# Performance work log

Measured on AMD Instinct MI355X. Metric: run time of the kernel, lower is better.

## Reference

```python
import jax, jax.numpy as jnp
import numpy as np

N = 50000
E = 800000
IN_DIM = 128
HEADS = 4
OUT_DIM = 32
TOT = HEADS * OUT_DIM  # 128 == IN_DIM -> residual_proj is None
LN_EPS = 1e-5
NEG_SLOPE = 0.2


def setup_inputs() -> dict:
    key = jax.random.key(0)
    ks = jax.random.split(key, 10)
    x = jax.random.normal(ks[0], (N, IN_DIM), dtype=jnp.float32)
    # random edges guaranteed src != dst (PyG GATv2Conv removes then re-adds self loops)
    src = jax.random.randint(ks[1], (E,), 0, N)
    off = jax.random.randint(ks[2], (E,), 1, N)
    dst = (src + off) % N
    edge_index = jnp.stack([src, dst]).astype(jnp.int64)
    # glorot-style init for weights
    sc = 1.0 / np.sqrt(IN_DIM)
    W_l = jax.random.uniform(ks[3], (IN_DIM, TOT), jnp.float32, -sc, sc)
    b_l = jnp.zeros((TOT,), jnp.float32)
    W_r = jax.random.uniform(ks[4], (IN_DIM, TOT), jnp.float32, -sc, sc)
    b_r = jnp.zeros((TOT,), jnp.float32)
    att = jax.random.uniform(ks[5], (HEADS, OUT_DIM), jnp.float32, -sc, sc)
    bias = jnp.zeros((TOT,), jnp.float32)
    ln_g = jnp.ones((TOT,), jnp.float32)
    ln_b = jnp.zeros((TOT,), jnp.float32)
    return {"x": x, "edge_index": edge_index, "W_l": W_l, "b_l": b_l,
            "W_r": W_r, "b_r": b_r, "att": att, "bias": bias,
            "ln_g": ln_g, "ln_b": ln_b}


def _gatv2_layer(x, src, dst, W_l, b_l, W_r, b_r, att, bias, ln_g, ln_b):
    n = x.shape[0]
    # GATv2Conv: x_l = lin_l(x) (source/messages), x_r = lin_r(x) (target)
    xl = (x @ W_l + b_l).reshape(n, HEADS, OUT_DIM)
    xr = (x @ W_r + b_r).reshape(n, HEADS, OUT_DIM)
    m = xl[src] + xr[dst]                               # [E+N, H, D]
    s = jnp.einsum('ehd,hd->eh', jax.nn.leaky_relu(m, NEG_SLOPE), att)
    # per-destination softmax (every node has a self loop -> no empty segments)
    smax = jax.ops.segment_max(s, dst, num_segments=n)  # [N, H]
    e = jnp.exp(s - smax[dst])
    denom = jax.ops.segment_sum(e, dst, num_segments=n)
    alpha = e / denom[dst]                              # [E+N, H]
    out = jax.ops.segment_sum(alpha[..., None] * xl[src], dst, num_segments=n)
    out = out.reshape(n, TOT) + bias
    out = out + x                                       # residual (in_dim == total_out_dim)
    mu = jnp.mean(out, axis=-1, keepdims=True)
    var = jnp.mean(jnp.square(out - mu), axis=-1, keepdims=True)
    y = (out - mu) / jnp.sqrt(var + LN_EPS) * ln_g + ln_b
    return jax.nn.elu(y)


def reference(x, edge_index, W_l, b_l, W_r, b_r, att, bias, ln_g, ln_b):
    n = x.shape[0]
    loops = jnp.arange(n, dtype=edge_index.dtype)
    src = jnp.concatenate([edge_index[0], loops])
    dst = jnp.concatenate([edge_index[1], loops])
    return _gatv2_layer(x, src, dst, W_l, b_l, W_r, b_r, att, bias, ln_g, ln_b)
```

## Files before the change

kernel.cpp:

```cpp
#include <hip/hip_runtime.h>

#define N_NODES 50000
#define E_EDGES 800000
#define M_TOTAL (E_EDGES + N_NODES)
#define IN_DIM 128
#define HEADS 4
#define OUT_DIM 32
#define TOT 128
#define LN_EPS 1e-5f
#define NEG_SLOPE 0.2f

#define SCAN_NBLK ((N_NODES + 255) / 256)
#define GEMM_NBLK ((N_NODES + 63) / 64)
#define CHUNK_NBLK ((M_TOTAL / 4 + 255) / 256)
#define HIST_NBLK 64
#define EPB 13312
#define HALF 25000

typedef __bf16 bf16x8 __attribute__((ext_vector_type(8)));
typedef float  f32x4  __attribute__((ext_vector_type(4)));
typedef _Float16 h2   __attribute__((ext_vector_type(2)));

__device__ __forceinline__ float quad_sum(float p) {
    p += __int_as_float(__builtin_amdgcn_update_dpp(
        0, __float_as_int(p), 0xB1 , 0xF, 0xF, true));
    p += __int_as_float(__builtin_amdgcn_update_dpp(
        0, __float_as_int(p), 0x4E , 0xF, 0xF, true));
    return p;
}

__global__ __launch_bounds__(256) void wthist_kernel(
    const int* __restrict__ dsts,
    const float* __restrict__ Wl, const float* __restrict__ Wr,
    unsigned* __restrict__ WT, unsigned char* __restrict__ H,
    unsigned char* __restrict__ rank8) {
    __shared__ unsigned cnt[HALF / 2];
    const int b = blockIdx.x, t = threadIdx.x;
    if (b < 64) {
        const int u = b * 256 + t;
        const int col = u >> 6, k2 = u & 63;
        const float* __restrict__ W = (col < 128) ? Wl : Wr;
        const int c = col & 127;
        union { __bf16 bb[2]; unsigned uu; } p;
        p.bb[0] = (__bf16)W[(2 * k2) * TOT + c];
        p.bb[1] = (__bf16)W[(2 * k2 + 1) * TOT + c];
        WT[col * 64 + k2] = p.uu;
        return;
    }
    const int hb = b - 64;
    const int m_begin = hb * EPB;
    const int m_end = min(m_begin + EPB, M_TOTAL);
    for (int pass = 0; pass < 2; ++pass) {
        const int lo = pass * HALF;
        for (int i = t; i < HALF / 2; i += 256) cnt[i] = 0;
        __syncthreads();
        for (int m0 = m_begin + t * 4; m0 < m_end; m0 += 1024) {
            int d[4];
            if (m0 < E_EDGES) {
                const int4 dv = *(const int4*)&dsts[m0];
                d[0] = dv.x; d[1] = dv.y; d[2] = dv.z; d[3] = dv.w;
            } else {
                d[0] = m0 - E_EDGES; d[1] = d[0] + 1; d[2] = d[0] + 2; d[3] = d[0] + 3;
            }
#pragma unroll
            for (int k = 0; k < 4; ++k) {
                const int dd = d[k] - lo;
                if ((unsigned)dd < (unsigned)HALF) {
                    const int sh = (dd & 1) * 16;
                    const unsigned old = atomicAdd(&cnt[dd >> 1], 1u << sh);
                    rank8[m0 + k] = (unsigned char)((old >> sh) & 0xffffu);
                }
            }
        }
        __syncthreads();
        unsigned* __restrict__ Hrow = (unsigned*)(H + (size_t)hb * N_NODES + lo);
        for (int i = t; i < HALF / 4; i += 256) {
            const unsigned w0 = cnt[2 * i], w1 = cnt[2 * i + 1];
            Hrow[i] = (w0 & 0xffu) | (((w0 >> 16) & 0xffu) << 8) |
                      ((w1 & 0xffu) << 16) | (((w1 >> 16) & 0xffu) << 24);
        }
        __syncthreads();
    }
}

__global__ __launch_bounds__(256) void scan1_kernel(
    const unsigned char* __restrict__ H, unsigned char* __restrict__ P,
    int* __restrict__ incl, int* __restrict__ blockSums,
    int* __restrict__ degtot) {
    __shared__ int sh[256];
    const int t = threadIdx.x;
    const int i = blockIdx.x * 256 + t;
    int tot = 0;
    if (i < N_NODES) {
        int run = 0;
#pragma unroll
        for (int b = 0; b < HIST_NBLK; ++b) {
            const int h = H[(size_t)b * N_NODES + i];
            P[(size_t)b * N_NODES + i] = (unsigned char)run;
            run += h;
        }
        tot = run;
        degtot[i] = tot;
    }
    sh[t] = tot;
    __syncthreads();
#pragma unroll
    for (int off = 1; off < 256; off <<= 1) {
        int u = (t >= off) ? sh[t - off] : 0;
        __syncthreads();
        sh[t] += u;
        __syncthreads();
    }
    if (i < N_NODES) incl[i] = sh[t];
    if (t == 255) blockSums[blockIdx.x] = sh[255];
}

__global__ __launch_bounds__(256) void scan23_kernel(
    const int* __restrict__ degtot, const int* __restrict__ blockSums,
    int* __restrict__ rowptr ) {
    __shared__ int sh[256];
    const int t = threadIdx.x;
    const int v0 = (t < SCAN_NBLK) ? blockSums[t] : 0;
    sh[t] = v0;
    __syncthreads();
#pragma unroll
    for (int off = 1; off < 256; off <<= 1) {
        int u = (t >= off) ? sh[t - off] : 0;
        __syncthreads();
        sh[t] += u;
        __syncthreads();
    }
    const int blockOff = (blockIdx.x == 0) ? 0 : sh[blockIdx.x - 1];
    const int i = blockIdx.x * 256 + t;
    if (i < N_NODES)
        rowptr[i] = blockOff + rowptr[i] - degtot[i];
    if (i == 0) rowptr[N_NODES] = M_TOTAL;
}

__global__ __launch_bounds__(256) void scattergemm_kernel(
    const int* __restrict__ srcs, const int* __restrict__ dsts,
    const int* __restrict__ rowptr, const unsigned char* __restrict__ P,
    const unsigned char* __restrict__ rank8,
    unsigned short* __restrict__ sorted16,
    const float* __restrict__ x, const unsigned* __restrict__ WT,
    const float* __restrict__ bl, const float* __restrict__ br,
    unsigned* __restrict__ xlb, unsigned* __restrict__ xrb) {
    if (blockIdx.x >= GEMM_NBLK) {
        const int sb = blockIdx.x - GEMM_NBLK;
        const int m0 = (sb * 256 + threadIdx.x) * 4;
        if (m0 >= M_TOTAL) return;
        int s[4], d[4];
        if (m0 < E_EDGES) {
            const int4 sv = *(const int4*)&srcs[m0];
            const int4 dv = *(const int4*)&dsts[m0];
            s[0] = sv.x; s[1] = sv.y; s[2] = sv.z; s[3] = sv.w;
            d[0] = dv.x; d[1] = dv.y; d[2] = dv.z; d[3] = dv.w;
        } else {
            s[0] = d[0] = m0 - E_EDGES;
            s[1] = d[1] = d[0] + 1; s[2] = d[2] = d[0] + 2; s[3] = d[3] = d[0] + 3;
        }
        const int hb = m0 / EPB;
        const unsigned char* __restrict__ Pb = P + (size_t)hb * N_NODES;
        const uchar4 r = *(const uchar4*)&rank8[m0];
        sorted16[rowptr[d[0]] + (int)Pb[d[0]] + (int)r.x] = (unsigned short)s[0];
        sorted16[rowptr[d[1]] + (int)Pb[d[1]] + (int)r.y] = (unsigned short)s[1];
        sorted16[rowptr[d[2]] + (int)Pb[d[2]] + (int)r.z] = (unsigned short)s[2];
        sorted16[rowptr[d[3]] + (int)Pb[d[3]] + (int)r.w] = (unsigned short)s[3];
        return;
    }
    __shared__ float epi[4][16][66];
    const int t = threadIdx.x, w = t >> 6, lane = t & 63;
    const int q = lane >> 4, ln = lane & 15;
    const int m0 = blockIdx.x * 64;

    const int row = min(m0 + w * 16 + ln, N_NODES - 1);
    const float* __restrict__ xrow = x + (size_t)row * IN_DIM;
    bf16x8 A[4];
#pragma unroll
    for (int c = 0; c < 4; ++c) {
        const float4 v0 = *(const float4*)&xrow[c * 32 + q * 8];
        const float4 v1 = *(const float4*)&xrow[c * 32 + q * 8 + 4];
        bf16x8 a;
        a[0] = (__bf16)v0.x; a[1] = (__bf16)v0.y; a[2] = (__bf16)v0.z; a[3] = (__bf16)v0.w;
        a[4] = (__bf16)v1.x; a[5] = (__bf16)v1.y; a[6] = (__bf16)v1.z; a[7] = (__bf16)v1.w;
        A[c] = a;
    }

    const int mr = lane >> 2, cg2 = (lane & 3) * 16;
    const int grow = m0 + w * 16 + mr;
#pragma unroll
    for (int g = 0; g < 4; ++g) {
        const int n0 = g * 64;
        const float* __restrict__ bvec = (g < 2) ? bl : br;
        f32x4 acc[4];
#pragma unroll
        for (int nt = 0; nt < 4; ++nt) {
            const float b = bvec[(n0 & 127) + nt * 16 + ln];
            acc[nt] = (f32x4){b, b, b, b};
        }
#pragma unroll
        for (int nt = 0; nt < 4; ++nt) {
            const int col = n0 + nt * 16 + ln;
#pragma unroll
            for (int c = 0; c < 4; ++c) {
                const bf16x8 B = *(const bf16x8*)&WT[col * 64 + c * 16 + q * 4];
                acc[nt] = __builtin_amdgcn_mfma_f32_16x16x32_bf16(A[c], B, acc[nt], 0, 0, 0);
            }
        }
#pragma unroll
        for (int nt = 0; nt < 4; ++nt)
#pragma unroll
            for (int r = 0; r < 4; ++r)
                epi[w][q * 4 + r][nt * 16 + ln] = acc[nt][r];

        if (grow < N_NODES) {
            unsigned p[8];
#pragma unroll
            for (int i = 0; i < 8; ++i) {
                union { _Float16 h[2]; unsigned u; } pk;
                pk.h[0] = (_Float16)epi[w][mr][cg2 + 2 * i];
                pk.h[1] = (_Float16)epi[w][mr][cg2 + 2 * i + 1];
                p[i] = pk.u;
            }
            unsigned* __restrict__ dst = ((g < 2) ? xlb : xrb) +
                (size_t)grow * 64 + (g & 1) * 32 + (cg2 >> 1);
            *(uint4*)&dst[0] = make_uint4(p[0], p[1], p[2], p[3]);
            *(uint4*)&dst[4] = make_uint4(p[4], p[5], p[6], p[7]);
        }
    }
}

__global__ __launch_bounds__(256) void gat_kernel(
    const int* __restrict__ rowptr, const unsigned short* __restrict__ sorted16,
    const unsigned* __restrict__ xlb, const unsigned* __restrict__ xrb,
    const float* __restrict__ att, const float* __restrict__ x,
    const float* __restrict__ bias, const float* __restrict__ g,
    const float* __restrict__ bvec, float* __restrict__ out) {
    const int d = blockIdx.x * 4 + (threadIdx.x >> 6);
    const int lane = threadIdx.x & 63;
    const int ln = lane & 15, q = lane >> 4;
    if (d >= N_NODES) return;

    h2 xrh[4], ath[4];
    {
        const uint4 ur = *(const uint4*)&xrb[(size_t)d * 64 + 4 * ln];
        union { uint4 u; h2 h[4]; } cr; cr.u = ur;
        xrh[0] = cr.h[0]; xrh[1] = cr.h[1]; xrh[2] = cr.h[2]; xrh[3] = cr.h[3];
        const float4 a0 = *(const float4*)&att[8 * ln];
        const float4 a1 = *(const float4*)&att[8 * ln + 4];
        ath[0][0] = (_Float16)a0.x; ath[0][1] = (_Float16)a0.y;
        ath[1][0] = (_Float16)a0.z; ath[1][1] = (_Float16)a0.w;
        ath[2][0] = (_Float16)a1.x; ath[2][1] = (_Float16)a1.y;
        ath[3][0] = (_Float16)a1.z; ath[3][1] = (_Float16)a1.w;
    }
    const h2 slope = (h2){(_Float16)NEG_SLOPE, (_Float16)NEG_SLOPE};
    const int beg = rowptr[d], end = rowptr[d + 1];

    float l = 0.f;
    h2 acc4[4];
#pragma unroll
    for (int k = 0; k < 4; ++k) acc4[k] = (h2){(_Float16)0.f, (_Float16)0.f};

    int s_b = (int)sorted16[min(beg + 4 + q, end - 1)];
    uint4 u;
    {
        const int s_a = (int)sorted16[min(beg + q, end - 1)];
        u = *(const uint4*)&xlb[(size_t)s_a * 64 + 4 * ln];
    }

    for (int base = beg; base < end; base += 4) {
        const int s_c = (int)sorted16[min(base + 8 + q, end - 1)];
        const uint4 u_next = *(const uint4*)&xlb[(size_t)s_b * 64 + 4 * ln];

        const bool valid = (base + q) < end;
        union { unsigned uu; h2 h; } c0, c1, c2, c3;
        c0.uu = u.x; c1.uu = u.y; c2.uu = u.z; c3.uu = u.w;
        h2 m0 = c0.h + xrh[0], m1 = c1.h + xrh[1];
        h2 m2 = c2.h + xrh[2], m3 = c3.h + xrh[3];
        m0 = __builtin_elementwise_max(m0, m0 * slope);
        m1 = __builtin_elementwise_max(m1, m1 * slope);
        m2 = __builtin_elementwise_max(m2, m2 * slope);
        m3 = __builtin_elementwise_max(m3, m3 * slope);
        float p = __builtin_amdgcn_fdot2(m0, ath[0], 0.0f, false);
        p = __builtin_amdgcn_fdot2(m1, ath[1], p, false);
        p = __builtin_amdgcn_fdot2(m2, ath[2], p, false);
        p = __builtin_amdgcn_fdot2(m3, ath[3], p, false);
        p = quad_sum(p);
        const float e = valid ? __expf(p) : 0.f;
        l += e;
        const _Float16 eh = (_Float16)e;
        const h2 e2 = (h2){eh, eh};
        acc4[0] += e2 * c0.h;
        acc4[1] += e2 * c1.h;
        acc4[2] += e2 * c2.h;
        acc4[3] += e2 * c3.h;

        u = u_next; s_b = s_c;
    }

#pragma unroll
    for (int off = 16; off <= 32; off <<= 1) {
        l += __shfl_xor(l, off, 64);
#pragma unroll
        for (int k = 0; k < 4; ++k) {
            union { h2 h; int i; } tmp; tmp.h = acc4[k];
            tmp.i = __shfl_xor(tmp.i, off, 64);
            acc4[k] += tmp.h;
        }
    }
    float acc[8];
#pragma unroll
    for (int k = 0; k < 4; ++k) {
        acc[2 * k]     = (float)acc4[k][0];
        acc[2 * k + 1] = (float)acc4[k][1];
    }

    const float inv_l = 1.0f / l;
    const float4 xv0 = *(const float4*)&x[(size_t)d * TOT + 8 * ln];
    const float4 xv1 = *(const float4*)&x[(size_t)d * TOT + 8 * ln + 4];
    const float4 bi0 = *(const float4*)&bias[8 * ln];
    const float4 bi1 = *(const float4*)&bias[8 * ln + 4];
    float v[8];
    v[0] = fmaf(acc[0], inv_l, bi0.x + xv0.x);
    v[1] = fmaf(acc[1], inv_l, bi0.y + xv0.y);
    v[2] = fmaf(acc[2], inv_l, bi0.z + xv0.z);
    v[3] = fmaf(acc[3], inv_l, bi0.w + xv0.w);
    v[4] = fmaf(acc[4], inv_l, bi1.x + xv1.x);
    v[5] = fmaf(acc[5], inv_l, bi1.y + xv1.y);
    v[6] = fmaf(acc[6], inv_l, bi1.z + xv1.z);
    v[7] = fmaf(acc[7], inv_l, bi1.w + xv1.w);
    float sum = 0.f, sq = 0.f;
#pragma unroll
    for (int k = 0; k < 8; ++k) { sum += v[k]; sq = fmaf(v[k], v[k], sq); }
#pragma unroll
    for (int off = 1; off <= 8; off <<= 1) {
        sum += __shfl_xor(sum, off, 64);
        sq  += __shfl_xor(sq,  off, 64);
    }
    const float mu  = sum * (1.0f / TOT);
    const float var = sq * (1.0f / TOT) - mu * mu;
    const float inv = rsqrtf(var + LN_EPS);
    const float4 g0 = *(const float4*)&g[8 * ln];
    const float4 g1 = *(const float4*)&g[8 * ln + 4];
    const float4 b0 = *(const float4*)&bvec[8 * ln];
    const float4 b1 = *(const float4*)&bvec[8 * ln + 4];
    float y[8];
    y[0] = (v[0] - mu) * inv * g0.x + b0.x;
    y[1] = (v[1] - mu) * inv * g0.y + b0.y;
    y[2] = (v[2] - mu) * inv * g0.z + b0.z;
    y[3] = (v[3] - mu) * inv * g0.w + b0.w;
    y[4] = (v[4] - mu) * inv * g1.x + b1.x;
    y[5] = (v[5] - mu) * inv * g1.y + b1.y;
    y[6] = (v[6] - mu) * inv * g1.z + b1.z;
    y[7] = (v[7] - mu) * inv * g1.w + b1.w;
#pragma unroll
    for (int k = 0; k < 8; ++k) y[k] = y[k] > 0.f ? y[k] : __expf(y[k]) - 1.f;
    if (q < 2) {
        float4 o = (q == 0) ? make_float4(y[0], y[1], y[2], y[3])
                            : make_float4(y[4], y[5], y[6], y[7]);
        *(float4*)&out[(size_t)d * TOT + 8 * ln + 4 * q] = o;
    }
}

extern "C" void kernel_launch(void* const* d_in, const int* in_sizes, int n_in,
                              void* d_out, int out_size, void* d_ws, size_t ws_size,
                              hipStream_t stream) {
    const float* x    = (const float*)d_in[0];
    const int*   ei   = (const int*)d_in[1];
    const float* Wl   = (const float*)d_in[2];
    const float* bl   = (const float*)d_in[3];
    const float* Wr   = (const float*)d_in[4];
    const float* br   = (const float*)d_in[5];
    const float* att  = (const float*)d_in[6];
    const float* bias = (const float*)d_in[7];
    const float* ln_g = (const float*)d_in[8];
    const float* ln_b = (const float*)d_in[9];
    const int* srcs = ei;
    const int* dsts = ei + E_EDGES;

    unsigned* xlb = (unsigned*)d_ws;
    unsigned* xrb = xlb + (size_t)N_NODES * 64;
    int*   degtot     = (int*)(xrb + (size_t)N_NODES * 64);
    int*   rowptr     = degtot + N_NODES;
    int*   blockSums  = rowptr + N_NODES + 1;
    unsigned* WT      = (unsigned*)(blockSums + SCAN_NBLK + 3);
    unsigned char* H  = (unsigned char*)(WT + 256 * 64);
    unsigned char* P  = H + (size_t)HIST_NBLK * N_NODES;
    unsigned short* sorted16 = (unsigned short*)(P + (size_t)HIST_NBLK * N_NODES);
    unsigned char*  rank8    = (unsigned char*)(sorted16 + M_TOTAL);

    wthist_kernel<<<64 + HIST_NBLK, 256, 0, stream>>>(dsts, Wl, Wr, WT, H, rank8);
    scan1_kernel<<<SCAN_NBLK, 256, 0, stream>>>(H, P, rowptr, blockSums, degtot);
    scan23_kernel<<<SCAN_NBLK, 256, 0, stream>>>(degtot, blockSums, rowptr);
    scattergemm_kernel<<<GEMM_NBLK + CHUNK_NBLK, 256, 0, stream>>>(
        srcs, dsts, rowptr, P, rank8, sorted16, x, WT, bl, br, xlb, xrb);
    gat_kernel<<<(N_NODES + 3) / 4, 256, 0, stream>>>(rowptr, sorted16, xlb, xrb, att, x,
                                                      bias, ln_g, ln_b, (float*)d_out);
}
```

Measured before the change: 195.5 us.

## Use 8-bit packed single-pass histogram, in-place scan, and 2x-unrolled edge loop

The histogram kernel now packs four 8-bit counters per LDS word, so all 50000 nodes fit in one pass instead of two 16-bit passes. The block count doubles to keep per-block counts below 256. The scan overwrites the histogram in place, dropping the separate P buffer. The gather loop in the attention kernel processes two groups of four edges per iteration with deeper prefetch, giving more memory-level parallelism. The costs are a larger LDS footprint (lower occupancy for the histogram blocks), twice as many histogram rows to scan, and higher register pressure in the gather loop.

```diff
diff --git a/kernel.cpp b/kernel.cpp
--- a/kernel.cpp
+++ b/kernel.cpp
@@ -13,9 +13,8 @@
 #define SCAN_NBLK ((N_NODES + 255) / 256)
 #define GEMM_NBLK ((N_NODES + 63) / 64)
 #define CHUNK_NBLK ((M_TOTAL / 4 + 255) / 256)
-#define HIST_NBLK 64
-#define EPB 13312
-#define HALF 25000
+#define HIST_NBLK 128
+#define EPB 6656
 
 typedef __bf16 bf16x8 __attribute__((ext_vector_type(8)));
 typedef float  f32x4  __attribute__((ext_vector_type(4)));
@@ -32,9 +31,9 @@
 __global__ __launch_bounds__(256) void wthist_kernel(
     const int* __restrict__ dsts,
     const float* __restrict__ Wl, const float* __restrict__ Wr,
-    unsigned* __restrict__ WT, unsigned char* __restrict__ H,
+    unsigned* __restrict__ WT, unsigned char* __restrict__ HP,
     unsigned char* __restrict__ rank8) {
-    __shared__ unsigned cnt[HALF / 2];
+    __shared__ unsigned cnt[N_NODES / 4];
     const int b = blockIdx.x, t = threadIdx.x;
     if (b < 64) {
         const int u = b * 256 + t;
@@ -50,41 +49,35 @@
     const int hb = b - 64;
     const int m_begin = hb * EPB;
     const int m_end = min(m_begin + EPB, M_TOTAL);
-    for (int pass = 0; pass < 2; ++pass) {
-        const int lo = pass * HALF;
-        for (int i = t; i < HALF / 2; i += 256) cnt[i] = 0;
-        __syncthreads();
-        for (int m0 = m_begin + t * 4; m0 < m_end; m0 += 1024) {
-            int d[4];
-            if (m0 < E_EDGES) {
-                const int4 dv = *(const int4*)&dsts[m0];
-                d[0] = dv.x; d[1] = dv.y; d[2] = dv.z; d[3] = dv.w;
-            } else {
-                d[0] = m0 - E_EDGES; d[1] = d[0] + 1; d[2] = d[0] + 2; d[3] = d[0] + 3;
-            }
-#pragma unroll
-            for (int k = 0; k < 4; ++k) {
-                const int dd = d[k] - lo;
-                if ((unsigned)dd < (unsigned)HALF) {
-                    const int sh = (dd & 1) * 16;
-                    const unsigned old = atomicAdd(&cnt[dd >> 1], 1u << sh);
-                    rank8[m0 + k] = (unsigned char)((old >> sh) & 0xffffu);
-                }
-            }
-        }
-        __syncthreads();
-        unsigned* __restrict__ Hrow = (unsigned*)(H + (size_t)hb * N_NODES + lo);
-        for (int i = t; i < HALF / 4; i += 256) {
-            const unsigned w0 = cnt[2 * i], w1 = cnt[2 * i + 1];
-            Hrow[i] = (w0 & 0xffu) | (((w0 >> 16) & 0xffu) << 8) |
-                      ((w1 & 0xffu) << 16) | (((w1 >> 16) & 0xffu) << 24);
-        }
-        __syncthreads();
-    }
+    for (int i = t; i < N_NODES / 4; i += 256) cnt[i] = 0;
+    __syncthreads();
+    for (int m0 = m_begin + t * 4; m0 < m_end; m0 += 1024) {
+        int d[4];
+        if (m0 < E_EDGES) {
+            const int4 dv = *(const int4*)&dsts[m0];
+            d[0] = dv.x; d[1] = dv.y; d[2] = dv.z; d[3] = dv.w;
+        } else {
+            d[0] = m0 - E_EDGES; d[1] = d[0] + 1; d[2] = d[0] + 2; d[3] = d[0] + 3;
+        }
+        uchar4 r;
+        unsigned old, sh;
+        sh = (d[0] & 3) * 8; old = atomicAdd(&cnt[d[0] >> 2], 1u << sh);
+        r.x = (unsigned char)(old >> sh);
+        sh = (d[1] & 3) * 8; old = atomicAdd(&cnt[d[1] >> 2], 1u << sh);
+        r.y = (unsigned char)(old >> sh);
+        sh = (d[2] & 3) * 8; old = atomicAdd(&cnt[d[2] >> 2], 1u << sh);
+        r.z = (unsigned char)(old >> sh);
+        sh = (d[3] & 3) * 8; old = atomicAdd(&cnt[d[3] >> 2], 1u << sh);
+        r.w = (unsigned char)(old >> sh);
+        *(uchar4*)&rank8[m0] = r;
+    }
+    __syncthreads();
+    unsigned* __restrict__ Hrow = (unsigned*)(HP + (size_t)hb * N_NODES);
+    for (int i = t; i < N_NODES / 4; i += 256) Hrow[i] = cnt[i];
 }
 
 __global__ __launch_bounds__(256) void scan1_kernel(
-    const unsigned char* __restrict__ H, unsigned char* __restrict__ P,
+    unsigned char* __restrict__ HP,
     int* __restrict__ incl, int* __restrict__ blockSums,
     int* __restrict__ degtot) {
     __shared__ int sh[256];
@@ -93,10 +86,10 @@
     int tot = 0;
     if (i < N_NODES) {
         int run = 0;
-#pragma unroll
+#pragma unroll 16
         for (int b = 0; b < HIST_NBLK; ++b) {
-            const int h = H[(size_t)b * N_NODES + i];
-            P[(size_t)b * N_NODES + i] = (unsigned char)run;
+            const int h = HP[(size_t)b * N_NODES + i];
+            HP[(size_t)b * N_NODES + i] = (unsigned char)run;
             run += h;
         }
         tot = run;
@@ -261,41 +254,58 @@
 #pragma unroll
     for (int k = 0; k < 4; ++k) acc4[k] = (h2){(_Float16)0.f, (_Float16)0.f};
 
-    int s_b = (int)sorted16[min(beg + 4 + q, end - 1)];
-    uint4 u;
+    uint4 u0, u1;
     {
-        const int s_a = (int)sorted16[min(beg + q, end - 1)];
-        u = *(const uint4*)&xlb[(size_t)s_a * 64 + 4 * ln];
-    }
-
-    for (int base = beg; base < end; base += 4) {
-        const int s_c = (int)sorted16[min(base + 8 + q, end - 1)];
-        const uint4 u_next = *(const uint4*)&xlb[(size_t)s_b * 64 + 4 * ln];
-
-        const bool valid = (base + q) < end;
-        union { unsigned uu; h2 h; } c0, c1, c2, c3;
-        c0.uu = u.x; c1.uu = u.y; c2.uu = u.z; c3.uu = u.w;
-        h2 m0 = c0.h + xrh[0], m1 = c1.h + xrh[1];
-        h2 m2 = c2.h + xrh[2], m3 = c3.h + xrh[3];
-        m0 = __builtin_elementwise_max(m0, m0 * slope);
-        m1 = __builtin_elementwise_max(m1, m1 * slope);
-        m2 = __builtin_elementwise_max(m2, m2 * slope);
-        m3 = __builtin_elementwise_max(m3, m3 * slope);
-        float p = __builtin_amdgcn_fdot2(m0, ath[0], 0.0f, false);
-        p = __builtin_amdgcn_fdot2(m1, ath[1], p, false);
-        p = __builtin_amdgcn_fdot2(m2, ath[2], p, false);
-        p = __builtin_amdgcn_fdot2(m3, ath[3], p, false);
-        p = quad_sum(p);
-        const float e = valid ? __expf(p) : 0.f;
-        l += e;
-        const _Float16 eh = (_Float16)e;
-        const h2 e2 = (h2){eh, eh};
-        acc4[0] += e2 * c0.h;
-        acc4[1] += e2 * c1.h;
-        acc4[2] += e2 * c2.h;
-        acc4[3] += e2 * c3.h;
-
-        u = u_next; s_b = s_c;
+        const int sA0 = (int)sorted16[min(beg + q, end - 1)];
+        const int sA1 = (int)sorted16[min(beg + 4 + q, end - 1)];
+        u0 = *(const uint4*)&xlb[(size_t)sA0 * 64 + 4 * ln];
+        u1 = *(const uint4*)&xlb[(size_t)sA1 * 64 + 4 * ln];
+    }
+    int sB0 = (int)sorted16[min(beg + 8 + q, end - 1)];
+    int sB1 = (int)sorted16[min(beg + 12 + q, end - 1)];
+
+    for (int base = beg; base < end; base += 8) {
+        const int sC0 = (int)sorted16[min(base + 16 + q, end - 1)];
+        const int sC1 = (int)sorted16[min(base + 20 + q, end - 1)];
+        const uint4 un0 = *(const uint4*)&xlb[(size_t)sB0 * 64 + 4 * ln];
+        const uint4 un1 = *(const uint4*)&xlb[(size_t)sB1 * 64 + 4 * ln];
+
+        union { unsigned uu; h2 h; } a0, a1, a2, a3, b0, b1, b2, b3;
+        a0.uu = u0.x; a1.uu = u0.y; a2.uu = u0.z; a3.uu = u0.w;
+        b0.uu = u1.x; b1.uu = u1.y; b2.uu = u1.z; b3.uu = u1.w;
+        h2 mA0 = a0.h + xrh[0], mA1 = a1.h + xrh[1];
+        h2 mA2 = a2.h + xrh[2], mA3 = a3.h + xrh[3];
+        h2 mB0 = b0.h + xrh[0], mB1 = b1.h + xrh[1];
+        h2 mB2 = b2.h + xrh[2], mB3 = b3.h + xrh[3];
+        mA0 = __builtin_elementwise_max(mA0, mA0 * slope);
+        mA1 = __builtin_elementwise_max(mA1, mA1 * slope);
+        mA2 = __builtin_elementwise_max(mA2, mA2 * slope);
+        mA3 = __builtin_elementwise_max(mA3, mA3 * slope);
+        mB0 = __builtin_elementwise_max(mB0, mB0 * slope);
+        mB1 = __builtin_elementwise_max(mB1, mB1 * slope);
+        mB2 = __builtin_elementwise_max(mB2, mB2 * slope);
+        mB3 = __builtin_elementwise_max(mB3, mB3 * slope);
+        float p0 = __builtin_amdgcn_fdot2(mA0, ath[0], 0.0f, false);
+        p0 = __builtin_amdgcn_fdot2(mA1, ath[1], p0, false);
+        p0 = __builtin_amdgcn_fdot2(mA2, ath[2], p0, false);
+        p0 = __builtin_amdgcn_fdot2(mA3, ath[3], p0, false);
+        float p1 = __builtin_amdgcn_fdot2(mB0, ath[0], 0.0f, false);
+        p1 = __builtin_amdgcn_fdot2(mB1, ath[1], p1, false);
+        p1 = __builtin_amdgcn_fdot2(mB2, ath[2], p1, false);
+        p1 = __builtin_amdgcn_fdot2(mB3, ath[3], p1, false);
+        p0 = quad_sum(p0);
+        p1 = quad_sum(p1);
+        const float e0 = (base + q < end) ? __expf(p0) : 0.f;
+        const float e1 = (base + 4 + q < end) ? __expf(p1) : 0.f;
+        l += e0 + e1;
+        const _Float16 eh0 = (_Float16)e0, eh1 = (_Float16)e1;
+        const h2 e20 = (h2){eh0, eh0}, e21 = (h2){eh1, eh1};
+        acc4[0] += e20 * a0.h; acc4[0] += e21 * b0.h;
+        acc4[1] += e20 * a1.h; acc4[1] += e21 * b1.h;
+        acc4[2] += e20 * a2.h; acc4[2] += e21 * b2.h;
+        acc4[3] += e20 * a3.h; acc4[3] += e21 * b3.h;
+
+        u0 = un0; u1 = un1; sB0 = sC0; sB1 = sC1;
     }
 
 #pragma unroll
@@ -384,16 +394,15 @@
     int*   rowptr     = degtot + N_NODES;
     int*   blockSums  = rowptr + N_NODES + 1;
     unsigned* WT      = (unsigned*)(blockSums + SCAN_NBLK + 3);
-    unsigned char* H  = (unsigned char*)(WT + 256 * 64);
-    unsigned char* P  = H + (size_t)HIST_NBLK * N_NODES;
-    unsigned short* sorted16 = (unsigned short*)(P + (size_t)HIST_NBLK * N_NODES);
+    unsigned char* HP = (unsigned char*)(WT + 256 * 64);
+    unsigned short* sorted16 = (unsigned short*)(HP + (size_t)HIST_NBLK * N_NODES);
     unsigned char*  rank8    = (unsigned char*)(sorted16 + M_TOTAL);
 
-    wthist_kernel<<<64 + HIST_NBLK, 256, 0, stream>>>(dsts, Wl, Wr, WT, H, rank8);
-    scan1_kernel<<<SCAN_NBLK, 256, 0, stream>>>(H, P, rowptr, blockSums, degtot);
+    wthist_kernel<<<64 + HIST_NBLK, 256, 0, stream>>>(dsts, Wl, Wr, WT, HP, rank8);
+    scan1_kernel<<<SCAN_NBLK, 256, 0, stream>>>(HP, rowptr, blockSums, degtot);
     scan23_kernel<<<SCAN_NBLK, 256, 0, stream>>>(degtot, blockSums, rowptr);
     scattergemm_kernel<<<GEMM_NBLK + CHUNK_NBLK, 256, 0, stream>>>(
-        srcs, dsts, rowptr, P, rank8, sorted16, x, WT, bl, br, xlb, xrb);
+        srcs, dsts, rowptr, HP, rank8, sorted16, x, WT, bl, br, xlb, xrb);
     gat_kernel<<<(N_NODES + 3) / 4, 256, 0, stream>>>(rowptr, sorted16, xlb, xrb, att, x,
                                                       bias, ln_g, ln_b, (float*)d_out);
 }
```

After: 185.7 us. 1.05x faster.
